# Optimization experiments

Measured on AMD Instinct MI355X. Metric: run time of the kernel, lower is better.

Reference implementation:

```python
import jax, jax.numpy as jnp
import numpy as np

N = 6144      # total atoms
F = 128       # hidden_dim
NB = 48       # number of molecules (batch segments)
LONG_RANGE_SCALE = 1.0


def setup_inputs() -> dict:
    key = jax.random.key(0)
    ks = jax.random.split(key, 16)
    s = 1.0 / np.sqrt(F)
    return {
        "h0": jax.random.normal(ks[0], (N, F), jnp.float32),
        "h1": jax.random.normal(ks[1], (N, 3, F), jnp.float32),
        "pos": jax.random.normal(ks[2], (N, 3), jnp.float32),
        "batch": jnp.sort(jax.random.randint(ks[3], (N,), 0, NB)),
        "qW1": jax.random.normal(ks[4], (F, F // 2), jnp.float32) * s,
        "qb1": jnp.zeros((F // 2,), jnp.float32),
        "qW2": jax.random.normal(ks[5], (F // 2, 1), jnp.float32) * s,
        "qb2": jnp.zeros((1,), jnp.float32),
        "cW1": jax.random.normal(ks[6], (F, F // 2), jnp.float32) * s,
        "cb1": jnp.zeros((F // 2,), jnp.float32),
        "cW2": jax.random.normal(ks[7], (F // 2, 1), jnp.float32) * s,
        "cb2": jnp.zeros((1,), jnp.float32),
        "muW": jax.random.normal(ks[8], (F, 1), jnp.float32) * s,
    }


def reference(h0, h1, pos, batch, qW1, qb1, qW2, qb2, cW1, cb1, cW2, cb2, muW):
    n = pos.shape[0]
    # pairwise geometry
    batch_mask = batch[:, None] == batch[None, :]                 # (N,N) bool
    diff = pos[:, None, :] - pos[None, :, :]                      # (N,N,3)
    dist_sq = jnp.sum(diff * diff, axis=-1)                       # (N,N)
    dist = jnp.sqrt(dist_sq + 1e-8)
    valid = batch_mask & ~jnp.eye(n, dtype=bool)
    validf = valid.astype(dist.dtype)

    energy = jnp.zeros((), dist.dtype)

    # --- Coulomb (use_charge) ---
    q = jax.nn.silu(h0 @ qW1 + qb1) @ qW2 + qb2                   # (N,1)
    q_sum = jax.ops.segment_sum(q, batch, num_segments=NB)        # (NB,1)
    cnt = jax.ops.segment_sum(jnp.ones((n, 1), q.dtype), batch, num_segments=NB)
    q_mean = q_sum / jnp.maximum(cnt, 1.0)                        # scatter_mean
    q = q - q_mean[batch]                                         # per-molecule neutrality
    qq = q @ q.T                                                  # (N,N)
    f_taper = 1.0 - jnp.exp(-0.5 * dist)
    E_coul = jnp.sum(qq / dist * f_taper * validf)
    energy = energy + 0.5 * E_coul * 14.399

    # --- van der Waals (use_vdw) ---
    c6 = jax.nn.softplus(jax.nn.silu(h0 @ cW1 + cb1) @ cW2 + cb2)  # (N,1), >0
    c6_ij = jnp.sqrt(c6 @ c6.T)                                    # (N,N)
    r6 = dist_sq ** 3
    E_vdw = -jnp.sum(c6_ij / (r6 + 20.0) * validf)
    energy = energy + 0.5 * E_vdw

    # --- dipole-dipole (use_dipole) ---
    mu = (h1 @ muW)[..., 0]                                        # (N,3)
    mu_dot_mu = mu @ mu.T                                          # (N,N)
    n_ij = diff / (dist[..., None] + 1e-8)                         # (N,N,3)
    mu_dot_n_i = jnp.einsum("id,ijd->ij", mu, n_ij)
    mu_dot_n_j = jnp.einsum("jd,ijd->ij", mu, n_ij)
    inv_r3 = 1.0 / (dist_sq * dist + 10.0)
    E_dip = jnp.sum((mu_dot_mu - 3.0 * mu_dot_n_i * mu_dot_n_j) * inv_r3 * validf)
    energy = energy + 0.5 * E_dip

    return energy * LONG_RANGE_SCALE
```

## Files before the change

kernel.cpp:

```cpp
#include <hip/hip_runtime.h>
#include <math.h>

#define F 128
#define H 64
#define AT 64
#define NBMOL 48
#define CAP 256
#define SPLIT 8

__device__ __forceinline__ float silu_f(float x) {
    return x / (1.0f + __expf(-x));
}
__device__ __forceinline__ float softplus_f(float x) {
    return fmaxf(x, 0.0f) + log1pf(__expf(-fabsf(x)));
}
__device__ __forceinline__ float frcp(float x) {
    return __builtin_amdgcn_rcpf(x);
}
__device__ __forceinline__ float dot4(float4 a, float4 b) {
    return fmaf(a.x, b.x, fmaf(a.y, b.y, fmaf(a.z, b.z, a.w * b.w)));
}

__global__ __launch_bounds__(256, 2) void k_mlp(
    const float* __restrict__ h0, const float* __restrict__ h1,
    const float* __restrict__ qW1, const float* __restrict__ qb1,
    const float* __restrict__ qW2, const float* __restrict__ qb2,
    const float* __restrict__ cW1, const float* __restrict__ cb1,
    const float* __restrict__ cW2, const float* __restrict__ cb2,
    const float* __restrict__ muW,
    float* __restrict__ q_raw, float* __restrict__ sqc6,
    float* __restrict__ mu,
    float* __restrict__ out, int N, int nrows)
{
    __shared__ float4 sW4[H * 32];
    __shared__ float4 sX4[AT * 32];
    __shared__ float red[4][AT];

    const int b = blockIdx.x;
    const int tid = threadIdx.x;
    if (b == 0 && tid == 0) out[0] = 0.0f;

    const int net  = b & 1;
    const int tile = b >> 1;
    const float* __restrict__ W1 = net ? cW1 : qW1;
    const float* __restrict__ b1 = net ? cb1 : qb1;
    const float* __restrict__ W2 = net ? cW2 : qW2;

    for (int idx = tid; idx < H * F; idx += 256) {
        int f = idx >> 6;
        int h = idx & 63;
        float val = W1[f * H + h];
        int f4 = f >> 2, fi = f & 3;
        ((float*)&sW4[h * 32 + (f4 ^ ((h >> 1) & 7))])[fi] = val;
    }
    const float4* __restrict__ h0v = (const float4*)h0;
    for (int idx = tid; idx < AT * 32; idx += 256) {
        int a = idx >> 5, f4 = idx & 31;
        int row = min(tile * AT + a, N - 1);
        sX4[a * 32 + (f4 ^ ((a >> 2) & 7))] = h0v[(size_t)row * 32 + f4];
    }
    __syncthreads();

    const int ag = tid & 15;
    const int hg = tid >> 4;

    float z[4][4];
    #pragma unroll
    for (int k = 0; k < 4; ++k) {
        float bv = b1[4 * hg + k];
        #pragma unroll
        for (int j = 0; j < 4; ++j) z[j][k] = bv;
    }

    #pragma unroll 4
    for (int f4 = 0; f4 < 32; ++f4) {
        float4 w[4];
        #pragma unroll
        for (int k = 0; k < 4; ++k) {
            int hr = 4 * hg + k;
            w[k] = sW4[hr * 32 + (f4 ^ ((hr >> 1) & 7))];
        }
        #pragma unroll
        for (int j = 0; j < 4; ++j) {
            int ar = 4 * ag + j;
            float4 x = sX4[ar * 32 + (f4 ^ ((ar >> 2) & 7))];
            #pragma unroll
            for (int k = 0; k < 4; ++k) z[j][k] += dot4(x, w[k]);
        }
    }

    float p[4];
    #pragma unroll
    for (int j = 0; j < 4; ++j) {
        p[j] = 0.f;
        #pragma unroll
        for (int k = 0; k < 4; ++k)
            p[j] = fmaf(silu_f(z[j][k]), W2[4 * hg + k], p[j]);
    }
    #pragma unroll
    for (int j = 0; j < 4; ++j) {
        p[j] += __shfl_xor(p[j], 16);
        p[j] += __shfl_xor(p[j], 32);
    }
    const int wv = tid >> 6, lane = tid & 63;
    if (lane < 16) {
        #pragma unroll
        for (int j = 0; j < 4; ++j) red[wv][4 * lane + j] = p[j];
    }
    __syncthreads();
    if (tid < AT) {
        float s = red[0][tid] + red[1][tid] + red[2][tid] + red[3][tid];
        int atom = tile * AT + tid;
        if (atom < N) {
            if (net == 0) q_raw[atom] = s + qb2[0];
            else          sqc6[atom]  = sqrtf(softplus_f(s + cb2[0]));
        }
    }

    const int slot = tid >> 4;
    const int l = tid & 15;
    const float4* mp = (const float4*)muW;
    const float4 m0 = mp[2 * l], m1 = mp[2 * l + 1];
    #pragma unroll
    for (int ppp = 0; ppp < 6; ++ppp) {
        int row = b * 96 + ppp * 16 + slot;
        if (row < nrows) {
            const float4* rp = (const float4*)(h1 + (size_t)row * F);
            float pm = dot4(rp[2 * l], m0) + dot4(rp[2 * l + 1], m1);
            #pragma unroll
            for (int off = 1; off < 16; off <<= 1) pm += __shfl_xor(pm, off);
            if (l == 0) mu[row] = pm;
        }
    }
}

__global__ __launch_bounds__(256) void k_pair(
    const float* __restrict__ pos,
    const int* __restrict__ batch,
    const float* __restrict__ q_raw, const float* __restrict__ sqc6,
    const float* __restrict__ mu,
    float* __restrict__ out, int N)
{
    const int b = blockIdx.x;
    const int s = blockIdx.y;
    const int tid = threadIdx.x;

    __shared__ int sst, sen;
    __shared__ float sq[CAP], sc[CAP], sp[3 * CAP], sm[3 * CAP];
    __shared__ float red[4];

    if (tid == 0) { sst = 0; sen = 0; }
    __syncthreads();
    for (int k = tid; k < N; k += 256) {
        int bk = batch[k];
        if (bk == b) {
            if (k == 0 || batch[k - 1] != b) sst = k;
            if (k == N - 1 || batch[k + 1] != b) sen = k + 1;
        }
    }
    __syncthreads();
    const int st = sst;
    const int n = sen - sst;

    float e_c = 0.f, e_v = 0.f, e_d = 0.f;

    if (n > 1 && n <= CAP) {
        float partsum = 0.f;
        for (int k = tid; k < n; k += 256) {
            float qv = q_raw[st + k];
            sq[k] = qv; partsum += qv;
            sc[k] = sqc6[st + k];
        }
        for (int k = tid; k < 3 * n; k += 256) {
            sp[k] = pos[3 * st + k];
            sm[k] = mu[3 * st + k];
        }
        #pragma unroll
        for (int off = 32; off > 0; off >>= 1)
            partsum += __shfl_xor(partsum, off);
        if ((tid & 63) == 0) red[tid >> 6] = partsum;
        __syncthreads();
        const float mean = (red[0] + red[1] + red[2] + red[3]) / (float)n;

        const int r = tid >> 4;
        const int c = tid & 15;
        for (int il = s + SPLIT * r; il < n; il += SPLIT * 16) {
            const float qi = sq[il] - mean;
            const float sci = sc[il];
            const float xi = sp[3 * il], yi = sp[3 * il + 1], zi = sp[3 * il + 2];
            const float mxi = sm[3 * il], myi = sm[3 * il + 1], mzi = sm[3 * il + 2];
            for (int jl = c; jl < n; jl += 16) {
                if (jl == il) continue;
                float dx = xi - sp[3 * jl], dy = yi - sp[3 * jl + 1],
                      dz = zi - sp[3 * jl + 2];
                float ds0 = fmaf(dx, dx, fmaf(dy, dy, dz * dz));
                float d = sqrtf(ds0 + 1e-8f);
                float inv_d = frcp(d);
                float qj = sq[jl] - mean;
                e_c = fmaf(qi * qj * inv_d, 1.0f - __expf(-0.5f * d), e_c);
                float r6 = ds0 * ds0 * ds0;
                e_v = fmaf(sci * sc[jl], frcp(r6 + 20.0f), e_v);
                float smx = sm[3 * jl], smy = sm[3 * jl + 1], smz = sm[3 * jl + 2];
                float mdm = fmaf(mxi, smx, fmaf(myi, smy, mzi * smz));
                float mdni = fmaf(mxi, dx, fmaf(myi, dy, mzi * dz)) * inv_d;
                float mdnj = fmaf(smx, dx, fmaf(smy, dy, smz * dz)) * inv_d;
                e_d = fmaf(mdm - 3.0f * mdni * mdnj,
                           frcp(fmaf(ds0, d, 10.0f)), e_d);
            }
        }
    } else if (n > CAP) {
        float partsum = 0.f;
        for (int k = tid; k < n; k += 256) partsum += q_raw[st + k];
        #pragma unroll
        for (int off = 32; off > 0; off >>= 1)
            partsum += __shfl_xor(partsum, off);
        if ((tid & 63) == 0) red[tid >> 6] = partsum;
        __syncthreads();
        const float mean = (red[0] + red[1] + red[2] + red[3]) / (float)n;
        const int r = tid >> 4, c = tid & 15;
        for (int j0 = 0; j0 < n; j0 += CAP) {
            const int chunk = min(CAP, n - j0);
            __syncthreads();
            for (int k = tid; k < chunk; k += 256) {
                sq[k] = q_raw[st + j0 + k];
                sc[k] = sqc6[st + j0 + k];
            }
            for (int k = tid; k < 3 * chunk; k += 256) {
                sp[k] = pos[3 * (st + j0) + k];
                sm[k] = mu[3 * (st + j0) + k];
            }
            __syncthreads();
            for (int il = s + SPLIT * r; il < n; il += SPLIT * 16) {
                const int i = st + il;
                const float qi = q_raw[i] - mean;
                const float sci = sqc6[i];
                const float xi = pos[i * 3], yi = pos[i * 3 + 1], zi = pos[i * 3 + 2];
                const float mxi = mu[i * 3], myi = mu[i * 3 + 1], mzi = mu[i * 3 + 2];
                for (int jl = c; jl < chunk; jl += 16) {
                    if (j0 + jl == il) continue;
                    float dx = xi - sp[3 * jl], dy = yi - sp[3 * jl + 1],
                          dz = zi - sp[3 * jl + 2];
                    float ds0 = fmaf(dx, dx, fmaf(dy, dy, dz * dz));
                    float d = sqrtf(ds0 + 1e-8f);
                    float inv_d = frcp(d);
                    float qj = sq[jl] - mean;
                    e_c = fmaf(qi * qj * inv_d, 1.0f - __expf(-0.5f * d), e_c);
                    float r6 = ds0 * ds0 * ds0;
                    e_v = fmaf(sci * sc[jl], frcp(r6 + 20.0f), e_v);
                    float smx = sm[3 * jl], smy = sm[3 * jl + 1], smz = sm[3 * jl + 2];
                    float mdm = fmaf(mxi, smx, fmaf(myi, smy, mzi * smz));
                    float mdni = fmaf(mxi, dx, fmaf(myi, dy, mzi * dz)) * inv_d;
                    float mdnj = fmaf(smx, dx, fmaf(smy, dy, smz * dz)) * inv_d;
                    e_d = fmaf(mdm - 3.0f * mdni * mdnj,
                               frcp(fmaf(ds0, d, 10.0f)), e_d);
                }
            }
        }
    }

    float vv = fmaf(7.1995f, e_c, fmaf(-0.5f, e_v, 0.5f * e_d));
    #pragma unroll
    for (int off = 32; off > 0; off >>= 1) vv += __shfl_xor(vv, off);
    __syncthreads();
    if ((tid & 63) == 0) red[tid >> 6] = vv;
    __syncthreads();
    if (tid == 0) atomicAdd(out, red[0] + red[1] + red[2] + red[3]);
}

extern "C" void kernel_launch(void* const* d_in, const int* in_sizes, int n_in,
                              void* d_out, int out_size, void* d_ws, size_t ws_size,
                              hipStream_t stream) {
    const float* h0  = (const float*)d_in[0];
    const float* h1  = (const float*)d_in[1];
    const float* pos = (const float*)d_in[2];
    const int*   batch = (const int*)d_in[3];
    const float* qW1 = (const float*)d_in[4];
    const float* qb1 = (const float*)d_in[5];
    const float* qW2 = (const float*)d_in[6];
    const float* qb2 = (const float*)d_in[7];
    const float* cW1 = (const float*)d_in[8];
    const float* cb1 = (const float*)d_in[9];
    const float* cW2 = (const float*)d_in[10];
    const float* cb2 = (const float*)d_in[11];
    const float* muW = (const float*)d_in[12];
    float* out = (float*)d_out;
    const int N = in_sizes[0] / F;

    float* ws = (float*)d_ws;
    float* q_raw = ws;
    float* sqc6  = q_raw + N;
    float* mu    = sqc6 + N;

    const int ntile = (N + AT - 1) / AT;
    const int nrows = 3 * N;

    k_mlp<<<2 * ntile, 256, 0, stream>>>(h0, h1, qW1, qb1, qW2, qb2,
                                         cW1, cb1, cW2, cb2, muW,
                                         q_raw, sqc6, mu, out, N, nrows);
    k_pair<<<dim3(NBMOL, SPLIT), 256, 0, stream>>>(pos, batch, q_raw, sqc6,
                                                   mu, out, N);
}
```

Before: 114.9 us.

## Fuse MLP and pairwise stages into one cooperative kernel with grid sync

Replaces the two-kernel launch (MLP, then pairwise energy) with a single cooperative kernel. Blocks first compute the charge/c6 MLPs and the dipole projections, then a grid-wide sync, then reuse all blocks (grid/48 splits per molecule) for the pairwise sums. The aim is to remove the second launch and the idle gap between kernels, and to spread pair work over more blocks. The cost is grid-sync overhead, a 64KB static shared buffer that may limit co-residency, and a fallback path to the old kernels if the cooperative launch fails.

```diff
diff --git a/kernel.cpp b/kernel.cpp
--- a/kernel.cpp
+++ b/kernel.cpp
@@ -1,5 +1,8 @@
 #include <hip/hip_runtime.h>
+#include <hip/hip_cooperative_groups.h>
 #include <math.h>
+
+namespace cg = cooperative_groups;
 
 #define F 128
 #define H 64
@@ -19,6 +22,222 @@
 }
 __device__ __forceinline__ float dot4(float4 a, float4 b) {
     return fmaf(a.x, b.x, fmaf(a.y, b.y, fmaf(a.z, b.z, a.w * b.w)));
+}
+
+__global__ __launch_bounds__(256, 2) void k_fused(
+    const float* __restrict__ h0, const float* __restrict__ h1,
+    const float* __restrict__ pos, const int* __restrict__ batch,
+    const float* __restrict__ qW1, const float* __restrict__ qb1,
+    const float* __restrict__ qW2, const float* __restrict__ qb2,
+    const float* __restrict__ cW1, const float* __restrict__ cb1,
+    const float* __restrict__ cW2, const float* __restrict__ cb2,
+    const float* __restrict__ muW,
+    float* __restrict__ q_raw, float* __restrict__ sqc6,
+    float* __restrict__ mu,
+    float* __restrict__ out, int N, int nmlp, int ndip, int splitp)
+{
+    __shared__ __align__(16) unsigned char smem[65536];
+    int*   sstp = (int*)(smem + 8192);
+    int*   senp = (int*)(smem + 8196);
+    float* redp = (float*)(smem + 8200);
+
+    const int b = blockIdx.x;
+    const int tid = threadIdx.x;
+    const int nrows = 3 * N;
+
+    if (b == 0 && tid == 0) out[0] = 0.0f;
+
+    if (b < nmlp) {
+        float4* sW4 = (float4*)smem;
+        float4* sX4 = (float4*)(smem + 32768);
+
+        const int net  = b & 1;
+        const int tile = b >> 1;
+        const float* __restrict__ W1 = net ? cW1 : qW1;
+        const float* __restrict__ b1 = net ? cb1 : qb1;
+        const float* __restrict__ W2 = net ? cW2 : qW2;
+
+        for (int idx = tid; idx < H * F; idx += 256) {
+            int f = idx >> 6;
+            int h = idx & 63;
+            float val = W1[f * H + h];
+            int f4 = f >> 2, fi = f & 3;
+            ((float*)&sW4[h * 32 + (f4 ^ ((h >> 1) & 7))])[fi] = val;
+        }
+        const float4* __restrict__ h0v = (const float4*)h0;
+        for (int idx = tid; idx < AT * 32; idx += 256) {
+            int a = idx >> 5, f4 = idx & 31;
+            int row = min(tile * AT + a, N - 1);
+            sX4[a * 32 + (f4 ^ ((a >> 2) & 7))] = h0v[(size_t)row * 32 + f4];
+        }
+        __syncthreads();
+
+        const int ag = tid & 15;
+        const int hg = tid >> 4;
+
+        float z[4][4];
+        #pragma unroll
+        for (int k = 0; k < 4; ++k) {
+            float bv = b1[4 * hg + k];
+            #pragma unroll
+            for (int j = 0; j < 4; ++j) z[j][k] = bv;
+        }
+
+        #pragma unroll 4
+        for (int f4 = 0; f4 < 32; ++f4) {
+            float4 w[4];
+            #pragma unroll
+            for (int k = 0; k < 4; ++k) {
+                int hr = 4 * hg + k;
+                w[k] = sW4[hr * 32 + (f4 ^ ((hr >> 1) & 7))];
+            }
+            #pragma unroll
+            for (int j = 0; j < 4; ++j) {
+                int ar = 4 * ag + j;
+                float4 x = sX4[ar * 32 + (f4 ^ ((ar >> 2) & 7))];
+                #pragma unroll
+                for (int k = 0; k < 4; ++k) z[j][k] += dot4(x, w[k]);
+            }
+        }
+
+        float p[4];
+        #pragma unroll
+        for (int j = 0; j < 4; ++j) {
+            p[j] = 0.f;
+            #pragma unroll
+            for (int k = 0; k < 4; ++k)
+                p[j] = fmaf(silu_f(z[j][k]), W2[4 * hg + k], p[j]);
+        }
+        #pragma unroll
+        for (int j = 0; j < 4; ++j) {
+            p[j] += __shfl_xor(p[j], 16);
+            p[j] += __shfl_xor(p[j], 32);
+        }
+        __syncthreads();
+        float* red = (float*)smem;
+        const int wv = tid >> 6, lane = tid & 63;
+        if (lane < 16) {
+            #pragma unroll
+            for (int j = 0; j < 4; ++j) red[wv * 64 + 4 * lane + j] = p[j];
+        }
+        __syncthreads();
+        if (tid < AT) {
+            float s = red[tid] + red[64 + tid] + red[128 + tid] + red[192 + tid];
+            int atom = tile * AT + tid;
+            if (atom < N) {
+                if (net == 0) q_raw[atom] = s + qb2[0];
+                else          sqc6[atom]  = sqrtf(softplus_f(s + cb2[0]));
+            }
+        }
+    } else if (b < nmlp + ndip) {
+        const int slot = tid >> 4;
+        const int l = tid & 15;
+        const float4* mp = (const float4*)muW;
+        const float4 m0 = mp[2 * l], m1 = mp[2 * l + 1];
+        const int r0 = (b - nmlp) * 64;
+        #pragma unroll
+        for (int pass = 0; pass < 4; ++pass) {
+            int row = r0 + pass * 16 + slot;
+            if (row < nrows) {
+                const float4* rp = (const float4*)(h1 + (size_t)row * F);
+                float pm = dot4(rp[2 * l], m0) + dot4(rp[2 * l + 1], m1);
+                #pragma unroll
+                for (int off = 1; off < 16; off <<= 1)
+                    pm += __shfl_xor(pm, off);
+                if (l == 0) mu[row] = pm;
+            }
+        }
+    }
+
+    cg::this_grid().sync();
+
+    const int mol = b % NBMOL;
+    const int s = b / NBMOL;
+
+    float* sq = (float*)smem;
+    float* sc = sq + CAP;
+    float* sp = sc + CAP;
+    float* sm = sp + 3 * CAP;
+
+    float e_c = 0.f, e_v = 0.f, e_d = 0.f;
+
+    if (s < splitp) {
+        if (tid == 0) { *sstp = 0; *senp = 0; }
+        __syncthreads();
+        for (int k = tid; k < N; k += 256) {
+            int bk = batch[k];
+            if (bk == mol) {
+                if (k == 0 || batch[k - 1] != mol) *sstp = k;
+                if (k == N - 1 || batch[k + 1] != mol) *senp = k + 1;
+            }
+        }
+        __syncthreads();
+        const int st = *sstp;
+        const int n = *senp - st;
+
+        if (n > 1 && n <= CAP) {
+            float partsum = 0.f;
+            for (int k = tid; k < n; k += 256) {
+                float qv = q_raw[st + k];
+                sq[k] = qv; partsum += qv;
+                sc[k] = sqc6[st + k];
+            }
+            for (int k = tid; k < 3 * n; k += 256) {
+                sp[k] = pos[3 * st + k];
+                sm[k] = mu[3 * st + k];
+            }
+            #pragma unroll
+            for (int off = 32; off > 0; off >>= 1)
+                partsum += __shfl_xor(partsum, off);
+            if ((tid & 63) == 0) redp[tid >> 6] = partsum;
+            __syncthreads();
+            const float mean = (redp[0] + redp[1] + redp[2] + redp[3]) / (float)n;
+
+            const int r = tid >> 4;
+            const int c = tid & 15;
+            for (int il = s + splitp * r; il < n; il += splitp * 16) {
+                const float qi = sq[il] - mean;
+                const float sci = sc[il];
+                const float xi = sp[3 * il], yi = sp[3 * il + 1],
+                            zi = sp[3 * il + 2];
+                const float mxi = sm[3 * il], myi = sm[3 * il + 1],
+                            mzi = sm[3 * il + 2];
+                for (int jl = c; jl < n; jl += 16) {
+                    if (jl == il) continue;
+                    float dx = xi - sp[3 * jl], dy = yi - sp[3 * jl + 1],
+                          dz = zi - sp[3 * jl + 2];
+                    float ds0 = fmaf(dx, dx, fmaf(dy, dy, dz * dz));
+                    float d = sqrtf(ds0 + 1e-8f);
+                    float inv_d = frcp(d);
+                    float qj = sq[jl] - mean;
+                    e_c = fmaf(qi * qj * inv_d, 1.0f - __expf(-0.5f * d), e_c);
+                    float r6 = ds0 * ds0 * ds0;
+                    e_v = fmaf(sci * sc[jl], frcp(r6 + 20.0f), e_v);
+                    float smx = sm[3 * jl], smy = sm[3 * jl + 1],
+                          smz = sm[3 * jl + 2];
+                    float mdm = fmaf(mxi, smx, fmaf(myi, smy, mzi * smz));
+                    float mdni = fmaf(mxi, dx, fmaf(myi, dy, mzi * dz)) * inv_d;
+                    float mdnj = fmaf(smx, dx, fmaf(smy, dy, smz * dz)) * inv_d;
+                    e_d = fmaf(mdm - 3.0f * mdni * mdnj,
+                               frcp(fmaf(ds0, d, 10.0f)), e_d);
+                }
+            }
+        }
+    } else {
+        __syncthreads();
+        __syncthreads();
+    }
+
+    float vv = fmaf(7.1995f, e_c, fmaf(-0.5f, e_v, 0.5f * e_d));
+    #pragma unroll
+    for (int off = 32; off > 0; off >>= 1) vv += __shfl_xor(vv, off);
+    __syncthreads();
+    if ((tid & 63) == 0) redp[tid >> 6] = vv;
+    __syncthreads();
+    if (tid == 0) {
+        float t = redp[0] + redp[1] + redp[2] + redp[3];
+        if (t != 0.0f) atomicAdd(out, t);
+    }
 }
 
 __global__ __launch_bounds__(256, 2) void k_mlp(
@@ -71,7 +290,6 @@
         #pragma unroll
         for (int j = 0; j < 4; ++j) z[j][k] = bv;
     }
-
     #pragma unroll 4
     for (int f4 = 0; f4 < 32; ++f4) {
         float4 w[4];
@@ -88,7 +306,6 @@
             for (int k = 0; k < 4; ++k) z[j][k] += dot4(x, w[k]);
         }
     }
-
     float p[4];
     #pragma unroll
     for (int j = 0; j < 4; ++j) {
@@ -284,19 +501,34 @@
     const float* cb2 = (const float*)d_in[11];
     const float* muW = (const float*)d_in[12];
     float* out = (float*)d_out;
-    const int N = in_sizes[0] / F;
+    int N = in_sizes[0] / F;
 
     float* ws = (float*)d_ws;
     float* q_raw = ws;
     float* sqc6  = q_raw + N;
     float* mu    = sqc6 + N;
 
-    const int ntile = (N + AT - 1) / AT;
-    const int nrows = 3 * N;
-
-    k_mlp<<<2 * ntile, 256, 0, stream>>>(h0, h1, qW1, qb1, qW2, qb2,
-                                         cW1, cb1, cW2, cb2, muW,
-                                         q_raw, sqc6, mu, out, N, nrows);
-    k_pair<<<dim3(NBMOL, SPLIT), 256, 0, stream>>>(pos, batch, q_raw, sqc6,
-                                                   mu, out, N);
-}
+    int ntile = (N + AT - 1) / AT;
+    int nmlp  = 2 * ntile;
+    int ndip  = (3 * N + 63) / 64;
+    int grid  = nmlp + ndip;
+    int splitp = grid / NBMOL;
+    int nrows = 3 * N;
+
+    void* args[] = {
+        (void*)&h0, (void*)&h1, (void*)&pos, (void*)&batch,
+        (void*)&qW1, (void*)&qb1, (void*)&qW2, (void*)&qb2,
+        (void*)&cW1, (void*)&cb1, (void*)&cW2, (void*)&cb2,
+        (void*)&muW, (void*)&q_raw, (void*)&sqc6, (void*)&mu,
+        (void*)&out, (void*)&N, (void*)&nmlp, (void*)&ndip, (void*)&splitp
+    };
+    hipError_t err = hipLaunchCooperativeKernel((void*)k_fused, dim3(grid),
+                                                dim3(256), args, 0, stream);
+    if (err != hipSuccess) {
+        k_mlp<<<nmlp, 256, 0, stream>>>(h0, h1, qW1, qb1, qW2, qb2,
+                                        cW1, cb1, cW2, cb2, muW,
+                                        q_raw, sqc6, mu, out, N, nrows);
+        k_pair<<<dim3(NBMOL, SPLIT), 256, 0, stream>>>(pos, batch, q_raw,
+                                                       sqc6, mu, out, N);
+    }
+}
```

New measurement: 177.5 us. +54.6%, slower.
